# Kernel optimization log

Hardware: AMD Instinct MI355X
Metric: run time of the kernel (lower is better)

## Reference

```python
import jax, jax.numpy as jnp
import numpy as np

B, S, D, H, O = 128, 1024, 64, 512, 1


def setup_inputs() -> dict:
    key = jax.random.key(0)
    ks = jax.random.split(key, 16)
    sc = 1.0 / np.sqrt(H)
    u = lambda k, shape: jax.random.uniform(k, shape, jnp.float32, -sc, sc)
    return {
        "x": jax.random.normal(ks[0], (B, S, D), jnp.float32),
        "W_ih0": u(ks[1], (4 * H, D)), "W_hh0": u(ks[2], (4 * H, H)),
        "b_ih0": u(ks[3], (4 * H,)), "b_hh0": u(ks[4], (4 * H,)),
        "W_ih1": u(ks[5], (4 * H, H)), "W_hh1": u(ks[6], (4 * H, H)),
        "b_ih1": u(ks[7], (4 * H,)), "b_hh1": u(ks[8], (4 * H,)),
        "W_a": u(ks[9], (H, H)), "b_a": u(ks[10], (H,)),
        "v_a": u(ks[11], (1, H)), "b_v": u(ks[12], (1,)),
        "fc_W": u(ks[13], (O, H)), "fc_b": u(ks[14], (O,)),
    }


def lstm_layer(x_sbd, W_ih, W_hh, b_ih, b_hh):
    # x_sbd: [S, B, Din] -> outputs [S, B, H]; PyTorch gate order i,f,g,o
    h0 = jnp.zeros((x_sbd.shape[1], W_hh.shape[1]), x_sbd.dtype)

    def step(carry, x_t):
        h, c = carry
        g = x_t @ W_ih.T + b_ih + h @ W_hh.T + b_hh
        i, f, gg, o = jnp.split(g, 4, axis=-1)
        c = jax.nn.sigmoid(f) * c + jax.nn.sigmoid(i) * jnp.tanh(gg)
        h = jax.nn.sigmoid(o) * jnp.tanh(c)
        return (h, c), h

    _, hs = jax.lax.scan(step, (h0, h0), x_sbd)
    return hs


def entmax15(x):
    # x: [B, S], normalization over axis 1 (faithful to the source's variant)
    n = x.shape[1]
    x = x - jnp.max(x, axis=1, keepdims=True)
    xs = jnp.flip(jnp.sort(x, axis=1), axis=1)  # descending
    csm = jnp.cumsum(xs, axis=1)
    rhos = jnp.arange(1, n + 1, dtype=x.dtype)
    support = rhos * xs - csm + 0.5
    support_thresh = support / rhos
    ssize = jnp.clip(jnp.sum(support > 0, axis=1, keepdims=True), 1, n - 1)
    tau = jnp.take_along_axis(support_thresh, ssize, axis=1)
    d = x - tau
    pos = d > 0
    y = jnp.where(pos, jnp.sqrt(jnp.where(pos, d, 1.0)), 0.0)
    return y / jnp.sum(y, axis=1, keepdims=True)


def reference(x, W_ih0, W_hh0, b_ih0, b_hh0, W_ih1, W_hh1, b_ih1, b_hh1,
              W_a, b_a, v_a, b_v, fc_W, fc_b):
    x_sbd = jnp.transpose(x, (1, 0, 2))  # [S, B, D]
    h1 = lstm_layer(x_sbd, W_ih0, W_hh0, b_ih0, b_hh0)
    h2 = lstm_layer(h1, W_ih1, W_hh1, b_ih1, b_hh1)
    lstm_out = jnp.transpose(h2, (1, 0, 2))  # [B, S, H]
    # additive attention energies: v_a(tanh(W_a(h)))
    e = jnp.einsum('bsh,oh->bso', jnp.tanh(jnp.einsum('bsh,gh->bsg', lstm_out, W_a) + b_a), v_a) + b_v
    att_weights = entmax15(e[..., 0])  # [B, S]
    context = jnp.einsum('bs,bsh->bh', att_weights, lstm_out)
    # dropout is identity in eval mode
    output = context @ fc_W.T + fc_b  # [B, O]
    return output, att_weights
```

## Files before the change

kernel.cpp:

```cpp
#include <hip/hip_runtime.h>

typedef __attribute__((ext_vector_type(8))) _Float16 half8;
typedef __attribute__((ext_vector_type(4))) float f32x4;
typedef __attribute__((ext_vector_type(4))) int   i32x4;

#define DEV static __device__ __forceinline__

DEV i32x4 mfma8i(i32x4 a, i32x4 b, i32x4 c){
  return __builtin_amdgcn_mfma_i32_16x16x64_i8(a, b, c, 0, 0, 0);
}
DEV void ld4(i32x4& d, const char* p){
  asm volatile("global_load_dwordx4 %0, %1, off sc0 sc1" : "=v"(d) : "v"(p));
}
DEV void st1(char* p, int v){
  asm volatile("global_store_byte %0, %1, off sc0 sc1" :: "v"(p), "v"(v) : "memory");
}
DEV void st_flag(unsigned int* p, unsigned int v){
  asm volatile("s_waitcnt vmcnt(0)" ::: "memory");
  asm volatile("global_store_dword %0, %1, off sc0 sc1" :: "v"(p), "v"(v) : "memory");
}
DEV void drain_vm(){ asm volatile("s_waitcnt vmcnt(0)" ::: "memory"); }
DEV void poll_ge(unsigned int* fp, unsigned int tgt){
  for (;;){
    unsigned int v = __hip_atomic_load(fp, __ATOMIC_RELAXED, __HIP_MEMORY_SCOPE_AGENT);
    if (__all(v >= tgt)) break;
    __builtin_amdgcn_s_sleep(1);
  }
}

DEV void str_h(const i32x4* W, const i32x4* B, i32x4* G){
  G[0]=mfma8i(W[0],B[0],G[0]);
  G[1]=mfma8i(W[0],B[1],G[1]); G[1]=mfma8i(W[1],B[0],G[1]);
  G[2]=mfma8i(W[0],B[2],G[2]); G[2]=mfma8i(W[1],B[1],G[2]); G[2]=mfma8i(W[2],B[0],G[2]);
  G[3]=mfma8i(W[0],B[3],G[3]); G[3]=mfma8i(W[1],B[2],G[3]); G[3]=mfma8i(W[2],B[1],G[3]); G[3]=mfma8i(W[3],B[0],G[3]);
  G[4]=mfma8i(W[0],B[4],G[4]); G[4]=mfma8i(W[1],B[3],G[4]); G[4]=mfma8i(W[2],B[2],G[4]); G[4]=mfma8i(W[3],B[1],G[4]); G[4]=mfma8i(W[4],B[0],G[4]);
  G[5]=mfma8i(W[1],B[4],G[5]); G[5]=mfma8i(W[2],B[3],G[5]); G[5]=mfma8i(W[3],B[2],G[5]); G[5]=mfma8i(W[4],B[1],G[5]);
}
DEV void str_x(const i32x4* W, const i32x4* X, i32x4* G){
  G[0]=mfma8i(W[0],X[0],G[0]);
  G[1]=mfma8i(W[0],X[1],G[1]); G[1]=mfma8i(W[1],X[0],G[1]);
  G[2]=mfma8i(W[0],X[2],G[2]); G[2]=mfma8i(W[1],X[1],G[2]); G[2]=mfma8i(W[2],X[0],G[2]);
  G[3]=mfma8i(W[0],X[3],G[3]); G[3]=mfma8i(W[1],X[2],G[3]); G[3]=mfma8i(W[2],X[1],G[3]); G[3]=mfma8i(W[3],X[0],G[3]);
  G[4]=mfma8i(W[0],X[4],G[4]); G[4]=mfma8i(W[1],X[3],G[4]); G[4]=mfma8i(W[2],X[2],G[4]); G[4]=mfma8i(W[3],X[1],G[4]); G[4]=mfma8i(W[4],X[0],G[4]);
  G[5]=mfma8i(W[0],X[5],G[5]); G[5]=mfma8i(W[1],X[4],G[5]); G[5]=mfma8i(W[2],X[3],G[5]); G[5]=mfma8i(W[3],X[2],G[5]); G[5]=mfma8i(W[4],X[1],G[5]);
}

#define SEG_STRIDE 4352
#define LDS_BYTES  (10 * SEG_STRIDE)

DEV void stage_half(char* const* hp, size_t tbase, int half, char* lds, int tid){
  const int row = tid >> 4;
  const int off = (tid & 15) * 16;
  i32x4 v[10];
  #pragma unroll
  for (int u = 0; u < 10; ++u){
    int plane = u >> 1, tile = u & 1;
    ld4(v[u], hp[plane] + tbase + (size_t)(tile * 16 + row) * 512 + (size_t)half * 256 + off);
  }
  asm volatile("s_waitcnt vmcnt(0)" ::: "memory");
  __builtin_amdgcn_sched_barrier(0);
  #pragma unroll
  for (int u = 0; u < 10; ++u)
    *(i32x4*)(lds + u * SEG_STRIDE + row * 272 + off) = v[u];
}

DEV void compute_half(const char* const* wp, size_t rowb, int wofs, int hc,
                      const char* lds, int l15, int l4, i32x4* Ga, i32x4* Gb){
  #pragma unroll
  for (int c = 0; c < 4; ++c){
    i32x4 Wc[5], Ba[5], Bb[5];
    #pragma unroll
    for (int p = 0; p < 5; ++p)
      Wc[p] = *(const i32x4*)(wp[p] + rowb + (size_t)(wofs + hc + c) * 64 + l4 * 16);
    #pragma unroll
    for (int p = 0; p < 5; ++p){
      Ba[p] = *(const i32x4*)(lds + (p * 2 + 0) * SEG_STRIDE + l15 * 272 + c * 64 + l4 * 16);
      Bb[p] = *(const i32x4*)(lds + (p * 2 + 1) * SEG_STRIDE + l15 * 272 + c * 64 + l4 * 16);
    }
    str_h(Wc, Ba, Ga);
    str_h(Wc, Bb, Gb);
  }
}

__global__ void k_prep_zero(unsigned int* cnt){
  cnt[threadIdx.x] = 0u;
}

DEV void wsplit5(float v, char* o1, char* o2, char* o3, char* o4, char* o5){
  float q1 = rintf(v * 0x1p11f);
  float r1 = fmaf(q1, -0x1p-11f, v);
  float q2 = rintf(r1 * 0x1p18f);
  float r2 = fmaf(q2, -0x1p-18f, r1);
  float q3 = rintf(r2 * 0x1p25f);
  float r3 = fmaf(q3, -0x1p-25f, r2);
  float q4 = rintf(r3 * 0x1p32f);
  float r4 = fmaf(q4, -0x1p-32f, r3);
  float q5 = rintf(r4 * 0x1p39f);
  *o1=(char)(int)q1; *o2=(char)(int)q2; *o3=(char)(int)q3;
  *o4=(char)(int)q4; *o5=(char)(int)q5;
}

__global__ void k_prep_w0(const float* __restrict__ Wih0, const float* __restrict__ Whh0,
                          char* __restrict__ p1, char* __restrict__ p2, char* __restrict__ p3,
                          char* __restrict__ p4, char* __restrict__ p5){
  int idx = blockIdx.x * 256 + threadIdx.x;
  int k = idx % 576;
  int r = (idx / 576) & 63;
  int j = idx / 36864;
  int R = (r & 3) * 512 + j * 16 + (r >> 2);
  float v = (k < 512) ? Whh0[(size_t)R * 512 + k] : Wih0[(size_t)R * 64 + (k - 512)];
  wsplit5(v, p1 + idx, p2 + idx, p3 + idx, p4 + idx, p5 + idx);
}

__global__ void k_prep_w1(const float* __restrict__ Wih1, const float* __restrict__ Whh1,
                          char* __restrict__ p1, char* __restrict__ p2, char* __restrict__ p3,
                          char* __restrict__ p4, char* __restrict__ p5){
  int idx = blockIdx.x * 256 + threadIdx.x;
  int k = idx & 1023;
  int r = (idx >> 10) & 63;
  int j = idx >> 16;
  int R = (r & 3) * 512 + j * 16 + (r >> 2);
  float v = (k < 512) ? Wih1[(size_t)R * 512 + k] : Whh1[(size_t)R * 512 + (k - 512)];
  wsplit5(v, p1 + idx, p2 + idx, p3 + idx, p4 + idx, p5 + idx);
}

__global__ void k_prep_b(const float* __restrict__ bih0, const float* __restrict__ bhh0,
                         const float* __restrict__ bih1, const float* __restrict__ bhh1,
                         double* __restrict__ bias0, double* __restrict__ bias1){
  int idx = blockIdx.x * 256 + threadIdx.x;
  int i2 = idx & 2047;
  int j = i2 >> 6, r = i2 & 63;
  int R = (r & 3) * 512 + j * 16 + (r >> 2);
  if (idx < 2048) bias0[i2] = (double)bih0[R] + (double)bhh0[R];
  else            bias1[i2] = (double)bih1[R] + (double)bhh1[R];
}

__global__ void k_prep_wa(const float* __restrict__ Wa,
                          char* __restrict__ p1, char* __restrict__ p2,
                          char* __restrict__ p3, char* __restrict__ p4){
  int idx = blockIdx.x * 256 + threadIdx.x;
  float v = Wa[idx];
  float q1 = rintf(v * 0x1p11f);
  float r1 = fmaf(q1, -0x1p-11f, v);
  float q2 = rintf(r1 * 0x1p18f);
  float r2 = fmaf(q2, -0x1p-18f, r1);
  float q3 = rintf(r2 * 0x1p25f);
  float r3 = fmaf(q3, -0x1p-25f, r2);
  float q4 = rintf(r3 * 0x1p32f);
  p1[idx]=(char)(int)q1; p2[idx]=(char)(int)q2;
  p3[idx]=(char)(int)q3; p4[idx]=(char)(int)q4;
}

DEV void hsplit5(double hd, char* o1, char* o2, char* o3, char* o4, char* o5){
  double q1 = rint(hd * 64.0);
  double r1 = hd - q1 * 0x1p-6;
  double q2 = rint(r1 * 0x1p13);
  double r2 = r1 - q2 * 0x1p-13;
  double q3 = rint(r2 * 0x1p20);
  double r3 = r2 - q3 * 0x1p-20;
  double q4 = rint(r3 * 0x1p27);
  double r4 = r3 - q4 * 0x1p-27;
  double q5 = rint(r4 * 0x1p34);
  *o1=(char)(int)q1; *o2=(char)(int)q2; *o3=(char)(int)q3;
  *o4=(char)(int)q4; *o5=(char)(int)q5;
}

DEV double sigd(double xv){ return 1.0 / (1.0 + exp(-xv)); }

__constant__ double SH_[6] = {0x1p-17, 0x1p-24, 0x1p-31, 0x1p-38, 0x1p-45, 0x1p-52};
__constant__ double SX_[6] = {0x1p-13, 0x1p-20, 0x1p-27, 0x1p-34, 0x1p-41, 0x1p-48};

__global__ __launch_bounds__(256, 1) void k_lstm_fused(
    const float* __restrict__ x,
    const char* w0p1, const char* w0p2, const char* w0p3, const char* w0p4, const char* w0p5,
    const double* __restrict__ bias0,
    const char* w1p1, const char* w1p2, const char* w1p3, const char* w1p4, const char* w1p5,
    const double* __restrict__ bias1,
    char* h1a, char* h1b, char* h1c, char* h1d, char* h1e,
    char* h2a, char* h2b, char* h2c, char* h2d, char* h2e,
    _Float16* __restrict__ h2h, char* __restrict__ h2l8,
    unsigned int* __restrict__ cnt)
{
  __shared__ char sbuf[LDS_BYTES];
  const int wg   = blockIdx.x;
  const int tid  = threadIdx.x;
  const int w    = tid >> 6;
  const int lane = tid & 63;
  const int l15  = lane & 15;
  const int l4   = lane >> 4;
  unsigned int* pflagL0 = cnt;
  unsigned int* pflagH2 = cnt + 128;

  const int isL1 = wg >= 128;
  const int wgl  = isL1 ? wg - 128 : wg;
  const int gi   = wgl >> 5;
  const int j    = wgl & 31;
  const int r0   = w * 16 + l15;
  const int b0   = gi * 32 + l15;
  const int b1   = b0 + 16;
  const int hid  = j * 16 + w * 4 + l4;
  const size_t ringmt0 = (size_t)b0 * 512;
  const size_t ringmt1 = (size_t)b1 * 512;
  const size_t gbase   = (size_t)(gi * 32) * 512;

  char* h1p[5] = {h1a, h1b, h1c, h1d, h1e};
  char* h2p[5] = {h2a, h2b, h2c, h2d, h2e};
  const i32x4 z = {0,0,0,0};

  if (!isL1){
    const char* wp[5] = {w0p1, w0p2, w0p3, w0p4, w0p5};
    const size_t rowb = ((size_t)j * 64 + r0) * 576;
    i32x4 WX[5];
    #pragma unroll
    for (int p = 0; p < 5; ++p)
      WX[p] = *(const i32x4*)(wp[p] + rowb + 8 * 64 + l4 * 16);
    double bsd[4];
    #pragma unroll
    for (int q = 0; q < 4; ++q) bsd[q] = bias0[j * 64 + w * 16 + l4 * 4 + q];
    double c0 = 0.0, c1 = 0.0;

    for (int t = 0; t < 1024; ++t){
      i32x4 XA[6], XB[6];
      {
        #pragma unroll
        for (int mt = 0; mt < 2; ++mt){
          const float* xr = x + ((size_t)(mt ? b1 : b0) * 1024 + t) * 64 + l4 * 16;
          unsigned int a[6][4] = {{0,0,0,0},{0,0,0,0},{0,0,0,0},{0,0,0,0},{0,0,0,0},{0,0,0,0}};
          #pragma unroll
          for (int i = 0; i < 16; ++i){
            float v = xr[i];
            float q1 = rintf(v * 4.0f);
            float r1 = fmaf(q1, -0.25f, v);
            float q2 = rintf(r1 * 0x1p9f);
            float r2 = fmaf(q2, -0x1p-9f, r1);
            float q3 = rintf(r2 * 0x1p16f);
            float r3 = fmaf(q3, -0x1p-16f, r2);
            float q4 = rintf(r3 * 0x1p23f);
            float r4 = fmaf(q4, -0x1p-23f, r3);
            float q5 = rintf(r4 * 0x1p30f);
            float r5 = fmaf(q5, -0x1p-30f, r4);
            float q6 = rintf(r5 * 0x1p37f);
            int wi = i >> 2, sh = (i & 3) * 8;
            a[0][wi] |= ((unsigned)(unsigned char)(char)(int)q1) << sh;
            a[1][wi] |= ((unsigned)(unsigned char)(char)(int)q2) << sh;
            a[2][wi] |= ((unsigned)(unsigned char)(char)(int)q3) << sh;
            a[3][wi] |= ((unsigned)(unsigned char)(char)(int)q4) << sh;
            a[4][wi] |= ((unsigned)(unsigned char)(char)(int)q5) << sh;
            a[5][wi] |= ((unsigned)(unsigned char)(char)(int)q6) << sh;
          }
          i32x4* X = mt ? XB : XA;
          #pragma unroll
          for (int p = 0; p < 6; ++p)
            X[p] = i32x4{(int)a[p][0], (int)a[p][1], (int)a[p][2], (int)a[p][3]};
        }
      }
      i32x4 Gha[6], Ghb[6], Gxa[6], Gxb[6];
      #pragma unroll
      for (int k = 0; k < 6; ++k){ Gha[k]=z; Ghb[k]=z; Gxa[k]=z; Gxb[k]=z; }
      str_x(WX, XA, Gxa);
      str_x(WX, XB, Gxb);

      if (w == 0 && lane < 32)
        poll_ge(pflagL0 + gi * 32 + lane, (unsigned)t);
      if (w == 1 && lane < 32 && t >= 8)
        poll_ge(pflagH2 + gi * 32 + lane, (unsigned)(t - 7));
      __syncthreads();

      if (t > 0){
        const size_t sb = ((size_t)((t - 1) & 7) << 16) + gbase;
        stage_half(h1p, sb, 0, sbuf, tid);
        __syncthreads();
        compute_half(wp, rowb, 0, 0, sbuf, l15, l4, Gha, Ghb);
        __syncthreads();
        stage_half(h1p, sb, 1, sbuf, tid);
        __syncthreads();
        compute_half(wp, rowb, 0, 4, sbuf, l15, l4, Gha, Ghb);
      }

      const size_t rb = (size_t)(t & 7) << 16;
      #pragma unroll
      for (int mt = 0; mt < 2; ++mt){
        i32x4* Gh = mt ? Ghb : Gha;
        i32x4* Gx = mt ? Gxb : Gxa;
        double g[4];
        #pragma unroll
        for (int q = 0; q < 4; ++q){
          double s = bsd[q];
          #pragma unroll
          for (int k = 0; k < 6; ++k)
            s += (double)Gh[k][q] * SH_[k] + (double)Gx[k][q] * SX_[k];
          g[q] = s;
        }
        double& cs = mt ? c1 : c0;
        cs = sigd(g[1]) * cs + sigd(g[0]) * tanh(g[2]);
        double hv = sigd(g[3]) * tanh(cs);
        size_t o = rb + (mt ? ringmt1 : ringmt0) + hid;
        char v1c, v2c, v3c, v4c, v5c;
        hsplit5(hv, &v1c, &v2c, &v3c, &v4c, &v5c);
        st1(h1p[0] + o, v1c); st1(h1p[1] + o, v2c); st1(h1p[2] + o, v3c);
        st1(h1p[3] + o, v4c); st1(h1p[4] + o, v5c);
      }

      drain_vm();
      __syncthreads();
      if (tid == 0) st_flag(pflagL0 + wgl, (unsigned)(t + 1));
    }
  } else {
    const char* wp[5] = {w1p1, w1p2, w1p3, w1p4, w1p5};
    const size_t rowb = ((size_t)j * 64 + r0) * 1024;
    double bsd[4];
    #pragma unroll
    for (int q = 0; q < 4; ++q) bsd[q] = bias1[j * 64 + w * 16 + l4 * 4 + q];
    double c0 = 0.0, c1 = 0.0;

    for (int t = 0; t < 1024; ++t){
      if (w == 0 && lane < 32)
        poll_ge(pflagL0 + gi * 32 + lane, (unsigned)(t + 1));
      __syncthreads();

      i32x4 Gha[6], Ghb[6];
      #pragma unroll
      for (int k = 0; k < 6; ++k){ Gha[k]=z; Ghb[k]=z; }
      {
        const size_t sb = ((size_t)(t & 7) << 16) + gbase;
        stage_half(h1p, sb, 0, sbuf, tid);
        __syncthreads();
        compute_half(wp, rowb, 0, 0, sbuf, l15, l4, Gha, Ghb);
        __syncthreads();
        stage_half(h1p, sb, 1, sbuf, tid);
        __syncthreads();
        compute_half(wp, rowb, 0, 4, sbuf, l15, l4, Gha, Ghb);
        __syncthreads();
      }

      if (t > 0){
        if (w == 0 && lane < 32)
          poll_ge(pflagH2 + gi * 32 + lane, (unsigned)t);
        __syncthreads();
        const size_t sb = ((size_t)((t - 1) & 3) << 16) + gbase;
        stage_half(h2p, sb, 0, sbuf, tid);
        __syncthreads();
        compute_half(wp, rowb, 8, 0, sbuf, l15, l4, Gha, Ghb);
        __syncthreads();
        stage_half(h2p, sb, 1, sbuf, tid);
        __syncthreads();
        compute_half(wp, rowb, 8, 4, sbuf, l15, l4, Gha, Ghb);
      }

      const size_t rb = (size_t)(t & 3) << 16;
      #pragma unroll
      for (int mt = 0; mt < 2; ++mt){
        i32x4* Gh = mt ? Ghb : Gha;
        double g[4];
        #pragma unroll
        for (int q = 0; q < 4; ++q){
          double s = bsd[q];
          #pragma unroll
          for (int k = 0; k < 6; ++k) s += (double)Gh[k][q] * SH_[k];
          g[q] = s;
        }
        double& cs = mt ? c1 : c0;
        cs = sigd(g[1]) * cs + sigd(g[0]) * tanh(g[2]);
        double hv = sigd(g[3]) * tanh(cs);
        size_t o = rb + (mt ? ringmt1 : ringmt0) + hid;
        char v1c, v2c, v3c, v4c, v5c;
        hsplit5(hv, &v1c, &v2c, &v3c, &v4c, &v5c);
        st1(h2p[0] + o, v1c); st1(h2p[1] + o, v2c); st1(h2p[2] + o, v3c);
        st1(h2p[3] + o, v4c); st1(h2p[4] + o, v5c);
        float hf = (float)hv;
        _Float16 hh = (_Float16)hf;
        float rs = hf - (float)hh;
        union { _Float16 h; unsigned short u; } cb; cb.h = hh;
        int E = (cb.u >> 10) & 31; if (E < 1) E = 1;
        int qr = (int)rintf(ldexpf(rs, 33 - E));
        qr = qr < -127 ? -127 : (qr > 127 ? 127 : qr);
        size_t pb = ((size_t)(mt ? b1 : b0) * 1024 + t) * 512 + hid;
        h2h[pb] = hh;
        h2l8[pb] = (char)qr;
      }

      drain_vm();
      __syncthreads();
      if (tid == 0) st_flag(pflagH2 + wgl, (unsigned)(t + 1));
    }
  }
}

__global__ __launch_bounds__(256) void k_att_e(
    const _Float16* __restrict__ h2, const char* __restrict__ h2l8,
    const char* __restrict__ wa1, const char* __restrict__ wa2,
    const char* __restrict__ wa3, const char* __restrict__ wa4,
    const float* __restrict__ b_a, const float* __restrict__ v_a,
    const float* __restrict__ b_v, double* __restrict__ e)
{
  __shared__ char Ap[4][32][528];
  __shared__ char Wp[2][4][16][528];
  __shared__ double partial[2][32];
  const int tid  = threadIdx.x;
  const int w    = tid >> 6;
  const int mt   = w & 1;
  const int nh   = w >> 1;
  const int lane = tid & 63;
  const int l15  = lane & 15;
  const int l4   = lane >> 4;
  const size_t rid0 = (size_t)blockIdx.x * 32;

  for (int i = tid; i < 2048; i += 256){
    int row = i >> 6, c8 = (i & 63) << 3;
    const _Float16* hp = h2 + (rid0 + row) * 512 + c8;
    const char*     rp = h2l8 + (rid0 + row) * 512 + c8;
    unsigned long long o1 = 0, o2 = 0, o3 = 0, o4 = 0;
    #pragma unroll
    for (int q = 0; q < 8; ++q){
      union { _Float16 h; unsigned short u; } cb; cb.h = hp[q];
      int E = (cb.u >> 10) & 31; if (E < 1) E = 1;
      float h = (float)cb.h + ldexpf((float)rp[q], E - 33);
      float q1 = rintf(h * 64.f);     float r1 = fmaf(q1, -0x1p-6f, h);
      float q2 = rintf(r1 * 0x1p13f); float r2 = fmaf(q2, -0x1p-13f, r1);
      float q3 = rintf(r2 * 0x1p20f); float r3 = fmaf(q3, -0x1p-20f, r2);
      float q4 = rintf(r3 * 0x1p27f);
      o1 |= ((unsigned long long)(unsigned char)(char)(int)q1) << (8 * q);
      o2 |= ((unsigned long long)(unsigned char)(char)(int)q2) << (8 * q);
      o3 |= ((unsigned long long)(unsigned char)(char)(int)q3) << (8 * q);
      o4 |= ((unsigned long long)(unsigned char)(char)(int)q4) << (8 * q);
    }
    *(unsigned long long*)&Ap[0][row][c8] = o1;
    *(unsigned long long*)&Ap[1][row][c8] = o2;
    *(unsigned long long*)&Ap[2][row][c8] = o3;
    *(unsigned long long*)&Ap[3][row][c8] = o4;
  }
  __syncthreads();

  const int sh = tid >> 7;
  const int st = tid & 127;
  double ep0 = 0.0, ep1 = 0.0, ep2 = 0.0, ep3 = 0.0;
  for (int it = 0; it < 16; ++it){
    if (it) __syncthreads();
    {
      int nt = sh * 16 + it;
      for (int i = st; i < 512; i += 128){
        int row = (i >> 5) & 15, c16 = (i & 31) << 4;
        size_t go = (size_t)(nt * 16 + row) * 512 + c16;
        *(i32x4*)&Wp[sh][0][row][c16] = *(const i32x4*)(wa1 + go);
        *(i32x4*)&Wp[sh][1][row][c16] = *(const i32x4*)(wa2 + go);
        *(i32x4*)&Wp[sh][2][row][c16] = *(const i32x4*)(wa3 + go);
        *(i32x4*)&Wp[sh][3][row][c16] = *(const i32x4*)(wa4 + go);
      }
    }
    __syncthreads();
    i32x4 G0={0,0,0,0},G1={0,0,0,0},G2={0,0,0,0},G3={0,0,0,0},G4={0,0,0,0},G5={0,0,0,0};
    #pragma unroll
    for (int c = 0; c < 8; ++c){
      int ko = c * 64 + l4 * 16;
      i32x4 A1 = *(const i32x4*)&Ap[0][mt * 16 + l15][ko];
      i32x4 A2 = *(const i32x4*)&Ap[1][mt * 16 + l15][ko];
      i32x4 A3 = *(const i32x4*)&Ap[2][mt * 16 + l15][ko];
      i32x4 A4 = *(const i32x4*)&Ap[3][mt * 16 + l15][ko];
      i32x4 B1 = *(const i32x4*)&Wp[nh][0][l15][ko];
      i32x4 B2 = *(const i32x4*)&Wp[nh][1][l15][ko];
      i32x4 B3 = *(const i32x4*)&Wp[nh][2][l15][ko];
      i32x4 B4 = *(const i32x4*)&Wp[nh][3][l15][ko];
      G0 = mfma8i(A1, B1, G0);
      G1 = mfma8i(A1, B2, G1); G1 = mfma8i(A2, B1, G1);
      G2 = mfma8i(A1, B3, G2); G2 = mfma8i(A2, B2, G2); G2 = mfma8i(A3, B1, G2);
      G3 = mfma8i(A1, B4, G3); G3 = mfma8i(A2, B3, G3); G3 = mfma8i(A3, B2, G3); G3 = mfma8i(A4, B1, G3);
      G4 = mfma8i(A2, B4, G4); G4 = mfma8i(A3, B3, G4); G4 = mfma8i(A4, B2, G4);
      G5 = mfma8i(A3, B4, G5); G5 = mfma8i(A4, B3, G5);
    }
    int n = (nh * 16 + it) * 16 + l15;
    double ban = (double)b_a[n], van = (double)v_a[n];
    #pragma unroll
    for (int q = 0; q < 4; ++q){
      double val = (double)G0[q]*SH_[0] + (double)G1[q]*SH_[1] + (double)G2[q]*SH_[2]
                 + (double)G3[q]*SH_[3] + (double)G4[q]*SH_[4] + (double)G5[q]*SH_[5] + ban;
      double tv = tanh(val) * van;
      if (q == 0) ep0 += tv; else if (q == 1) ep1 += tv;
      else if (q == 2) ep2 += tv; else ep3 += tv;
    }
  }
  #pragma unroll
  for (int m = 1; m < 16; m <<= 1){
    ep0 += __shfl_xor(ep0, m); ep1 += __shfl_xor(ep1, m);
    ep2 += __shfl_xor(ep2, m); ep3 += __shfl_xor(ep3, m);
  }
  if (l15 == 0){
    int rbase = mt * 16 + l4 * 4;
    partial[nh][rbase + 0] = ep0;
    partial[nh][rbase + 1] = ep1;
    partial[nh][rbase + 2] = ep2;
    partial[nh][rbase + 3] = ep3;
  }
  __syncthreads();
  if (tid < 32)
    e[rid0 + tid] = partial[0][tid] + partial[1][tid] + (double)b_v[0];
}

__global__ __launch_bounds__(256) void k_entmax(
    const double* __restrict__ e, const _Float16* __restrict__ h2,
    const float* __restrict__ fcW, const float* __restrict__ fcb,
    float* __restrict__ out)
{
  __shared__ double xu[1024], sbd[1024], t0d[1024], t1d[1024];
  __shared__ float sbf[1024];
  __shared__ float red4[4];
  __shared__ double redd[4];
  __shared__ double scald;
  const int tid  = threadIdx.x;
  const int b    = blockIdx.x;
  const int wv   = tid >> 6;
  const int lane = tid & 63;

  double lm = -1e300;
  for (int i = tid; i < 1024; i += 256){
    double v = e[b * 1024 + i];
    xu[i] = v;
    lm = fmax(lm, v);
  }
  for (int m = 32; m >= 1; m >>= 1) lm = fmax(lm, __shfl_xor(lm, m));
  if (lane == 0) redd[wv] = lm;
  __syncthreads();
  double rowmax = fmax(fmax(redd[0], redd[1]), fmax(redd[2], redd[3]));
  __syncthreads();
  for (int i = tid; i < 1024; i += 256){
    double v = xu[i] - rowmax;
    xu[i] = v; sbd[i] = v;
  }
  __syncthreads();

  for (int ksz = 2; ksz <= 1024; ksz <<= 1){
    for (int jj = ksz >> 1; jj > 0; jj >>= 1){
      for (int i = tid; i < 1024; i += 256){
        int ixj = i ^ jj;
        if (ixj > i){
          double a = sbd[i], c = sbd[ixj];
          if (((i & ksz) == 0) ? (a > c) : (a < c)){ sbd[i] = c; sbd[ixj] = a; }
        }
      }
      __syncthreads();
    }
  }

  for (int i = tid; i < 1024; i += 256) t0d[i] = sbd[1023 - i];
  __syncthreads();
  double* src = t0d; double* dst = t1d;
  for (int off = 1; off < 1024; off <<= 1){
    for (int i = tid; i < 1024; i += 256)
      dst[i] = src[i] + ((i >= off) ? src[i - off] : 0.0);
    __syncthreads();
    double* tmp = src; src = dst; dst = tmp;
  }

  float lc = 0.f;
  for (int i = tid; i < 1024; i += 256){
    double xs_i = sbd[1023 - i];
    double sup = (double)(i + 1) * xs_i - src[i] + 0.5;
    if (sup > 0.0) lc += 1.f;
  }
  for (int m = 32; m >= 1; m >>= 1) lc += __shfl_xor(lc, m);
  if (lane == 0) red4[wv] = lc;
  __syncthreads();
  if (tid == 0){
    int cntS = (int)(red4[0] + red4[1] + red4[2] + red4[3] + 0.5f);
    int ss = cntS < 1 ? 1 : (cntS > 1023 ? 1023 : cntS);
    double xss = sbd[1023 - ss];
    scald = ((double)(ss + 1) * xss - src[ss] + 0.5) / (double)(ss + 1);
  }
  __syncthreads();
  double tau = scald;

  double ls = 0.0;
  for (int i = tid; i < 1024; i += 256){
    double d = xu[i] - tau;
    double y = (d > 0.0) ? sqrt(d) : 0.0;
    dst[i] = y;
    ls += y;
  }
  for (int m = 32; m >= 1; m >>= 1) ls += __shfl_xor(ls, m);
  if (lane == 0) redd[wv] = ls;
  __syncthreads();
  double Z = redd[0] + redd[1] + redd[2] + redd[3];
  __syncthreads();
  for (int i = tid; i < 1024; i += 256){
    float a = (float)(dst[i] / Z);
    sbf[i] = a;
    out[128 + b * 1024 + i] = a;
  }
  __syncthreads();

  const int h0 = tid * 2;
  float cx0 = 0.f, cx1 = 0.f;
  for (int s = 0; s < 1024; ++s){
    float wt = sbf[s];
    if (wt > 0.f){
      unsigned int u = *(const unsigned int*)(h2 + ((size_t)b * 1024 + s) * 512 + h0);
      union { unsigned int u; _Float16 h[2]; } cv; cv.u = u;
      cx0 += wt * (float)cv.h[0];
      cx1 += wt * (float)cv.h[1];
    }
  }
  float p = fcW[h0] * cx0 + fcW[h0 + 1] * cx1;
  for (int m = 32; m >= 1; m >>= 1) p += __shfl_xor(p, m);
  if (lane == 0) red4[wv] = p;
  __syncthreads();
  if (tid == 0) out[b] = red4[0] + red4[1] + red4[2] + red4[3] + fcb[0];
}

extern "C" void kernel_launch(void* const* d_in, const int* in_sizes, int n_in,
                              void* d_out, int out_size, void* d_ws, size_t ws_size,
                              hipStream_t stream)
{
  (void)in_sizes; (void)n_in; (void)out_size;
  const float* x    = (const float*)d_in[0];
  const float* Wih0 = (const float*)d_in[1];
  const float* Whh0 = (const float*)d_in[2];
  const float* bih0 = (const float*)d_in[3];
  const float* bhh0 = (const float*)d_in[4];
  const float* Wih1 = (const float*)d_in[5];
  const float* Whh1 = (const float*)d_in[6];
  const float* bih1 = (const float*)d_in[7];
  const float* bhh1 = (const float*)d_in[8];
  const float* Wa   = (const float*)d_in[9];
  const float* ba   = (const float*)d_in[10];
  const float* va   = (const float*)d_in[11];
  const float* bv   = (const float*)d_in[12];
  const float* fcW  = (const float*)d_in[13];
  const float* fcb  = (const float*)d_in[14];

  const size_t NEED = 223773696ull;
  if (ws_size < NEED) return;

  char* ws = (char*)d_ws;
  unsigned int* cnt = (unsigned int*)(ws);
  char* w0p[5]; for (int p = 0; p < 5; ++p) w0p[p] = ws + 1024ull + (size_t)p * 1179648ull;
  double* bias0 = (double*)(ws + 5899264ull);
  char* w1p[5]; for (int p = 0; p < 5; ++p) w1p[p] = ws + 5915648ull + (size_t)p * 2097152ull;
  double* bias1 = (double*)(ws + 16401408ull);
  char* wa1 = ws + 16417792ull;
  char* wa2 = wa1 + 262144ull;
  char* wa3 = wa2 + 262144ull;
  char* wa4 = wa3 + 262144ull;
  char* h1p[5]; for (int p = 0; p < 5; ++p) h1p[p] = ws + 17466368ull + (size_t)p * 524288ull;
  char* h2p[5]; for (int p = 0; p < 5; ++p) h2p[p] = ws + 20087808ull + (size_t)p * 262144ull;
  double* ebuf = (double*)(ws + 21398528ull);
  _Float16* h2h = (_Float16*)(ws + 22447104ull);
  char* h2l8 = ws + 156664832ull;
  float* out = (float*)d_out;

  k_prep_zero<<<1, 256, 0, stream>>>(cnt);
  k_prep_w0<<<4608, 256, 0, stream>>>(Wih0, Whh0, w0p[0], w0p[1], w0p[2], w0p[3], w0p[4]);
  k_prep_w1<<<8192, 256, 0, stream>>>(Wih1, Whh1, w1p[0], w1p[1], w1p[2], w1p[3], w1p[4]);
  k_prep_b<<<16, 256, 0, stream>>>(bih0, bhh0, bih1, bhh1, bias0, bias1);
  k_prep_wa<<<1024, 256, 0, stream>>>(Wa, wa1, wa2, wa3, wa4);
  k_lstm_fused<<<256, 256, 0, stream>>>(x,
      w0p[0], w0p[1], w0p[2], w0p[3], w0p[4], bias0,
      w1p[0], w1p[1], w1p[2], w1p[3], w1p[4], bias1,
      h1p[0], h1p[1], h1p[2], h1p[3], h1p[4],
      h2p[0], h2p[1], h2p[2], h2p[3], h2p[4],
      h2h, h2l8, cnt);
  k_att_e<<<4096, 256, 0, stream>>>(h2h, h2l8, wa1, wa2, wa3, wa4, ba, va, bv, ebuf);
  k_entmax<<<128, 256, 0, stream>>>(ebuf, h2h, fcW, fcb, out);
}
```

Measured before the change: 21.63 ms.

## Stage full hidden vector per step and merge flag polls into one wave

Hidden-state staging now loads both halves (20 segments) into registers at once and writes them to a doubled LDS buffer. This removes the half/half stage-compute-sync sequence and several barriers per timestep. The layer-1 path issues the h1 and h2 loads together and waits only on the first batch before computing, so the h2 load latency overlaps the first matmul. Both flag polls are merged into a single wave using all 64 lanes. The cost is higher register pressure (up to 40 i32x4 live values) and twice the LDS, which could reduce occupancy or cause spills.

```diff
diff --git a/kernel.cpp b/kernel.cpp
--- a/kernel.cpp
+++ b/kernel.cpp
@@ -46,36 +46,39 @@
 }
 
 #define SEG_STRIDE 4352
-#define LDS_BYTES  (10 * SEG_STRIDE)
-
-DEV void stage_half(char* const* hp, size_t tbase, int half, char* lds, int tid){
+#define NSEG 20
+#define LDS_BYTES  (NSEG * SEG_STRIDE)
+
+DEV void stage_issue(char* const* hp, size_t tbase, i32x4* v, int tid){
   const int row = tid >> 4;
   const int off = (tid & 15) * 16;
-  i32x4 v[10];
   #pragma unroll
-  for (int u = 0; u < 10; ++u){
-    int plane = u >> 1, tile = u & 1;
+  for (int u = 0; u < NSEG; ++u){
+    int plane = u >> 2, tile = (u >> 1) & 1, half = u & 1;
     ld4(v[u], hp[plane] + tbase + (size_t)(tile * 16 + row) * 512 + (size_t)half * 256 + off);
   }
-  asm volatile("s_waitcnt vmcnt(0)" ::: "memory");
-  __builtin_amdgcn_sched_barrier(0);
+}
+DEV void stage_write(const i32x4* v, char* lds, int tid){
+  const int row = tid >> 4;
+  const int off = (tid & 15) * 16;
   #pragma unroll
-  for (int u = 0; u < 10; ++u)
+  for (int u = 0; u < NSEG; ++u)
     *(i32x4*)(lds + u * SEG_STRIDE + row * 272 + off) = v[u];
 }
 
-DEV void compute_half(const char* const* wp, size_t rowb, int wofs, int hc,
+DEV void compute_full(const char* const* wp, size_t rowb, int wofs,
                       const char* lds, int l15, int l4, i32x4* Ga, i32x4* Gb){
   #pragma unroll
-  for (int c = 0; c < 4; ++c){
+  for (int c = 0; c < 8; ++c){
+    const int half = c >> 2, cc = c & 3;
     i32x4 Wc[5], Ba[5], Bb[5];
     #pragma unroll
     for (int p = 0; p < 5; ++p)
-      Wc[p] = *(const i32x4*)(wp[p] + rowb + (size_t)(wofs + hc + c) * 64 + l4 * 16);
+      Wc[p] = *(const i32x4*)(wp[p] + rowb + (size_t)(wofs + c) * 64 + l4 * 16);
     #pragma unroll
     for (int p = 0; p < 5; ++p){
-      Ba[p] = *(const i32x4*)(lds + (p * 2 + 0) * SEG_STRIDE + l15 * 272 + c * 64 + l4 * 16);
-      Bb[p] = *(const i32x4*)(lds + (p * 2 + 1) * SEG_STRIDE + l15 * 272 + c * 64 + l4 * 16);
+      Ba[p] = *(const i32x4*)(lds + (p * 4 + 0 + half) * SEG_STRIDE + l15 * 272 + cc * 64 + l4 * 16);
+      Bb[p] = *(const i32x4*)(lds + (p * 4 + 2 + half) * SEG_STRIDE + l15 * 272 + cc * 64 + l4 * 16);
     }
     str_h(Wc, Ba, Ga);
     str_h(Wc, Bb, Gb);
@@ -260,21 +263,24 @@
       str_x(WX, XA, Gxa);
       str_x(WX, XB, Gxb);
 
-      if (w == 0 && lane < 32)
-        poll_ge(pflagL0 + gi * 32 + lane, (unsigned)t);
-      if (w == 1 && lane < 32 && t >= 8)
-        poll_ge(pflagH2 + gi * 32 + lane, (unsigned)(t - 7));
+      if (w == 0){
+        unsigned int* fp = (lane < 32) ? (pflagL0 + gi * 32 + lane)
+                                       : (pflagH2 + gi * 32 + (lane - 32));
+        unsigned int tgt = (lane < 32) ? (unsigned)t
+                          : ((t >= 8) ? (unsigned)(t - 7) : 0u);
+        poll_ge(fp, tgt);
+      }
       __syncthreads();
 
       if (t > 0){
+        i32x4 A[NSEG];
         const size_t sb = ((size_t)((t - 1) & 7) << 16) + gbase;
-        stage_half(h1p, sb, 0, sbuf, tid);
+        stage_issue(h1p, sb, A, tid);
+        drain_vm();
+        __builtin_amdgcn_sched_barrier(0);
+        stage_write(A, sbuf, tid);
         __syncthreads();
-        compute_half(wp, rowb, 0, 0, sbuf, l15, l4, Gha, Ghb);
-        __syncthreads();
-        stage_half(h1p, sb, 1, sbuf, tid);
-        __syncthreads();
-        compute_half(wp, rowb, 0, 4, sbuf, l15, l4, Gha, Ghb);
+        compute_full(wp, rowb, 0, sbuf, l15, l4, Gha, Ghb);
       }
 
       const size_t rb = (size_t)(t & 7) << 16;
@@ -314,37 +320,41 @@
     double c0 = 0.0, c1 = 0.0;
 
     for (int t = 0; t < 1024; ++t){
-      if (w == 0 && lane < 32)
-        poll_ge(pflagL0 + gi * 32 + lane, (unsigned)(t + 1));
+      if (w == 0){
+        unsigned int* fp = (lane < 32) ? (pflagL0 + gi * 32 + lane)
+                                       : (pflagH2 + gi * 32 + (lane - 32));
+        unsigned int tgt = (lane < 32) ? (unsigned)(t + 1)
+                          : ((t > 0) ? (unsigned)t : 0u);
+        poll_ge(fp, tgt);
+      }
       __syncthreads();
 
       i32x4 Gha[6], Ghb[6];
       #pragma unroll
       for (int k = 0; k < 6; ++k){ Gha[k]=z; Ghb[k]=z; }
-      {
-        const size_t sb = ((size_t)(t & 7) << 16) + gbase;
-        stage_half(h1p, sb, 0, sbuf, tid);
+
+      i32x4 A[NSEG], Bv[NSEG];
+      const size_t sbA = ((size_t)(t & 7) << 16) + gbase;
+      stage_issue(h1p, sbA, A, tid);
+      if (t > 0){
+        const size_t sbB = ((size_t)((t - 1) & 3) << 16) + gbase;
+        stage_issue(h2p, sbB, Bv, tid);
+        asm volatile("s_waitcnt vmcnt(20)" ::: "memory");
+      } else {
+        drain_vm();
+      }
+      __builtin_amdgcn_sched_barrier(0);
+      stage_write(A, sbuf, tid);
+      __syncthreads();
+      compute_full(wp, rowb, 0, sbuf, l15, l4, Gha, Ghb);
+      __syncthreads();
+
+      if (t > 0){
+        drain_vm();
+        __builtin_amdgcn_sched_barrier(0);
+        stage_write(Bv, sbuf, tid);
         __syncthreads();
-        compute_half(wp, rowb, 0, 0, sbuf, l15, l4, Gha, Ghb);
-        __syncthreads();
-        stage_half(h1p, sb, 1, sbuf, tid);
-        __syncthreads();
-        compute_half(wp, rowb, 0, 4, sbuf, l15, l4, Gha, Ghb);
-        __syncthreads();
-      }
-
-      if (t > 0){
-        if (w == 0 && lane < 32)
-          poll_ge(pflagH2 + gi * 32 + lane, (unsigned)t);
-        __syncthreads();
-        const size_t sb = ((size_t)((t - 1) & 3) << 16) + gbase;
-        stage_half(h2p, sb, 0, sbuf, tid);
-        __syncthreads();
-        compute_half(wp, rowb, 8, 0, sbuf, l15, l4, Gha, Ghb);
-        __syncthreads();
-        stage_half(h2p, sb, 1, sbuf, tid);
-        __syncthreads();
-        compute_half(wp, rowb, 8, 4, sbuf, l15, l4, Gha, Ghb);
+        compute_full(wp, rowb, 8, sbuf, l15, l4, Gha, Ghb);
       }
 
       const size_t rb = (size_t)(t & 3) << 16;
```

Result: faster. 19.41 ms (-10.3%).
